# Kernel tuning notes

Hardware: AMD Instinct MI355X
Metric: run time of the kernel (lower is better)

Reference implementation:

```python
import jax, jax.numpy as jnp
import numpy as np

N_EMBD = 1024
N_HEAD = 16
HEAD_SIZE = 64


def setup_inputs() -> dict:
    key = jax.random.key(0)
    ks = jax.random.split(key, 6)
    B, T, C, H, D = 2, 2048, N_EMBD, N_HEAD, HEAD_SIZE
    s = 1.0 / np.sqrt(C)
    x = jax.random.normal(ks[0], (B, T, C), dtype=jnp.float32)
    Wq = jax.random.normal(ks[1], (H, C, D), dtype=jnp.float32) * s
    Wk = jax.random.normal(ks[2], (H, C, D), dtype=jnp.float32) * s
    Wv = jax.random.normal(ks[3], (H, C, D), dtype=jnp.float32) * s
    Wo = jax.random.normal(ks[4], (H * D, C), dtype=jnp.float32) * (1.0 / np.sqrt(H * D))
    bo = jax.random.normal(ks[5], (C,), dtype=jnp.float32) * 0.01
    return {"x": x, "Wq": Wq, "Wk": Wk, "Wv": Wv, "Wo": Wo, "bo": bo}


def reference(x, Wq, Wk, Wv, Wo, bo):
    B, T, C = x.shape
    H, _, D = Wq.shape
    # Per-head projections, batched across heads: [B,H,T,D]
    q = jnp.einsum('btc,hcd->bhtd', x, Wq)
    k = jnp.einsum('btc,hcd->bhtd', x, Wk)
    v = jnp.einsum('btc,hcd->bhtd', x, Wv)
    # NOTE: original scales by sqrt(C) = sqrt(n_embd), not sqrt(head_size)
    scale = 1.0 / jnp.sqrt(jnp.float32(C))
    att = jnp.einsum('bhtd,bhsd->bhts', q, k) * scale  # [B,H,T,T]
    causal = jnp.tril(jnp.ones((T, T), dtype=bool))
    att = jnp.where(causal, att, -jnp.inf)
    att = jax.nn.softmax(att, axis=-1)
    # dropout omitted (eval mode / deterministic reference)
    out = jnp.einsum('bhts,bhsd->bhtd', att, v)  # [B,H,T,D]
    out = out.transpose(0, 2, 1, 3).reshape(B, T, H * D)
    return out @ Wo + bo
```

## Files before the change

kernel.cpp:

```cpp
#include <hip/hip_runtime.h>
#include <hip/hip_bf16.h>


typedef __hip_bfloat16 bf16;
typedef __bf16 v8bf __attribute__((ext_vector_type(8)));
typedef float  v4f  __attribute__((ext_vector_type(4)));
typedef _Float16 v4h __attribute__((ext_vector_type(4)));
typedef unsigned long long u64;
typedef unsigned int u32;

#define MFMA16(a, b, c) __builtin_amdgcn_mfma_f32_16x16x32_bf16((a), (b), (c), 0, 0, 0)
#define MFMAH(a, b, c)  __builtin_amdgcn_mfma_f32_16x16x16f16((a), (b), (c), 0, 0, 0)

__device__ __forceinline__ bf16 f2b(float x) { return __float2bfloat16(x); }
__device__ __forceinline__ __bf16 f2braw(float x) {
  bf16 t = __float2bfloat16(x);
  return *reinterpret_cast<__bf16*>(&t);
}
__device__ __forceinline__ unsigned short f2bu(float x) {
  bf16 t = __float2bfloat16(x);
  return *reinterpret_cast<unsigned short*>(&t);
}
__device__ __forceinline__ unsigned short f2hu(float x) {
  _Float16 t = (_Float16)x;
  return *reinterpret_cast<unsigned short*>(&t);
}

__device__ __forceinline__ void load16_lds(const void* gptr, const void* lptr) {
  __builtin_amdgcn_global_load_lds(
      (const __attribute__((address_space(1))) u32*)gptr,
      (__attribute__((address_space(3))) u32*)lptr, 16, 0, 0);
}

__global__ __launch_bounds__(256) void prep_kernel(
    const float* __restrict__ x,
    const float* __restrict__ Wq, const float* __restrict__ Wk,
    const float* __restrict__ Wv, const float* __restrict__ Wo,
    bf16* __restrict__ xb, bf16* __restrict__ wt, bf16* __restrict__ wot)
{
  __shared__ float Lt[32][33];
  const int bid = blockIdx.x, tid = threadIdx.x;

  if (bid < 2048) {
    size_t i = ((size_t)bid * 256 + tid) * 8;
    float4 f0 = *(const float4*)(x + i);
    float4 f1 = *(const float4*)(x + i + 4);
    v8bf v;
    v[0] = f2braw(f0.x); v[1] = f2braw(f0.y); v[2] = f2braw(f0.z); v[3] = f2braw(f0.w);
    v[4] = f2braw(f1.x); v[5] = f2braw(f1.y); v[6] = f2braw(f1.z); v[7] = f2braw(f1.w);
    *(v8bf*)(xb + i) = v;
    return;
  }
  const int tx = tid & 31, ty = tid >> 5;
  if (bid < 5120) {
    const int idx = bid - 2048;
    const int z = idx >> 6, rem = idx & 63;
    const int p = z >> 4, h = z & 15;
    const float* ib = ((p == 0) ? Wq : (p == 1) ? Wk : Wv) + (size_t)h * 65536;
    bf16* ob = wt + (size_t)z * 65536;
    const int j0 = (rem & 1) * 32, i0 = (rem >> 1) * 32;
    #pragma unroll
    for (int r = 0; r < 4; ++r)
      Lt[ty + 8 * r][tx] = ib[(size_t)(i0 + ty + 8 * r) * 64 + j0 + tx];
    __syncthreads();
    #pragma unroll
    for (int r = 0; r < 4; ++r)
      ob[(size_t)(j0 + ty + 8 * r) * 1024 + i0 + tx] = f2b(Lt[tx][ty + 8 * r]);
  } else {
    const int idx = bid - 5120;
    const int j0 = (idx & 31) * 32, i0 = (idx >> 5) * 32;
    #pragma unroll
    for (int r = 0; r < 4; ++r)
      Lt[ty + 8 * r][tx] = Wo[(size_t)(i0 + ty + 8 * r) * 1024 + j0 + tx];
    __syncthreads();
    #pragma unroll
    for (int r = 0; r < 4; ++r)
      wot[(size_t)(j0 + ty + 8 * r) * 1024 + i0 + tx] = f2b(Lt[tx][ty + 8 * r]);
  }
}

__global__ __launch_bounds__(256) void qkv_gemm_kernel(
    const bf16* __restrict__ xb, const bf16* __restrict__ wt,
    bf16* __restrict__ qkv)
{
  __shared__ __align__(16) bf16 Ash[2][128][32];
  __shared__ __align__(16) bf16 Bsh[2][128][32];

  const int mt = blockIdx.x, nt = blockIdx.y;
  const int tid = threadIdx.x, w = tid >> 6, lane = tid & 63;
  const int ln = lane & 15, quad = lane >> 4;
  const int wm = w >> 1, wn = w & 1;
  const int m0 = mt * 128, n0 = nt * 128;

  const v4f vzero = {0.f, 0.f, 0.f, 0.f};
  v4f acc[4][4];
  #pragma unroll
  for (int mf = 0; mf < 4; ++mf)
    #pragma unroll
    for (int nf = 0; nf < 4; ++nf) acc[mf][nf] = vzero;

  const int srow = lane >> 2, sseg = (lane & 3) * 8;
  const bf16* ga = xb + (size_t)(m0 + 32 * w + srow) * 1024 + sseg;
  const bf16* gb = wt + (size_t)(n0 + 32 * w + srow) * 1024 + sseg;

  {
    load16_lds(ga,             &Ash[0][32 * w][0]);
    load16_lds(ga + 16 * 1024, &Ash[0][32 * w + 16][0]);
    load16_lds(gb,             &Bsh[0][32 * w][0]);
    load16_lds(gb + 16 * 1024, &Bsh[0][32 * w + 16][0]);
  }

  for (int kt = 0; kt < 32; ++kt) {
    const int buf = kt & 1;
    __syncthreads();

    if (kt < 31) {
      const int k0 = (kt + 1) * 32, nb = buf ^ 1;
      load16_lds(ga + k0,             &Ash[nb][32 * w][0]);
      load16_lds(ga + 16 * 1024 + k0, &Ash[nb][32 * w + 16][0]);
      load16_lds(gb + k0,             &Bsh[nb][32 * w][0]);
      load16_lds(gb + 16 * 1024 + k0, &Bsh[nb][32 * w + 16][0]);
    }

    v8bf af[4], bfv[4];
    #pragma unroll
    for (int mf = 0; mf < 4; ++mf)
      af[mf] = *(const v8bf*)&Ash[buf][wm * 64 + mf * 16 + ln][quad * 8];
    #pragma unroll
    for (int nf = 0; nf < 4; ++nf)
      bfv[nf] = *(const v8bf*)&Bsh[buf][wn * 64 + nf * 16 + ln][quad * 8];

    #pragma unroll
    for (int mf = 0; mf < 4; ++mf)
      #pragma unroll
      for (int nf = 0; nf < 4; ++nf)
        acc[mf][nf] = MFMA16(af[mf], bfv[nf], acc[mf][nf]);
  }

  const int jcol0 = n0 + wn * 64;
  const int p = jcol0 >> 10;
  const int h = (jcol0 >> 6) & 15;
  const float scale = (p == 0) ? 0.03125f : 1.0f;

  if (p < 2) {
    bf16* base = qkv + (size_t)p * 4194304 + (size_t)h * 262144;
    #pragma unroll
    for (int mf = 0; mf < 4; ++mf)
      #pragma unroll
      for (int nf = 0; nf < 4; ++nf) {
        int d = nf * 16 + ln;
        #pragma unroll
        for (int r = 0; r < 4; ++r) {
          int m = m0 + wm * 64 + mf * 16 + quad * 4 + r;
          base[(size_t)m * 64 + d] = f2b(acc[mf][nf][r] * scale);
        }
      }
  } else {
    _Float16* vb = (_Float16*)(qkv + (size_t)2 * 4194304 + (size_t)h * 262144);
    #pragma unroll
    for (int mf = 0; mf < 4; ++mf) {
      int mrow = m0 + wm * 64 + mf * 16 + quad * 4;
      int bi = mrow >> 11, t0 = mrow & 2047;
      #pragma unroll
      for (int nf = 0; nf < 4; ++nf) {
        int d = nf * 16 + ln;
        u64 pk = (u64)f2hu(acc[mf][nf][0]) |
                 ((u64)f2hu(acc[mf][nf][1]) << 16) |
                 ((u64)f2hu(acc[mf][nf][2]) << 32) |
                 ((u64)f2hu(acc[mf][nf][3]) << 48);
        *(u64*)(vb + (size_t)bi * 131072 + (size_t)d * 2048 + t0) = pk;
      }
    }
  }
}

__global__ __launch_bounds__(128) void attn_kernel(
    const bf16* __restrict__ qkv, bf16* __restrict__ att)
{
  __shared__ __align__(16) bf16     Ksh[2][2][64][32];
  __shared__ __align__(16) _Float16 Vsh[2][4][64][16];

  const int fid = blockIdx.x;
  const int mtraw = fid & 31;
  const int mt = ((fid >> 8) & 1) ? (31 - mtraw) : mtraw;
  const int grp = (fid >> 5) & 31;
  const int b = grp >> 4, h = grp & 15;
  const int row0 = mt * 64;

  const int tid = threadIdx.x, w = tid >> 6, lane = tid & 63;
  const int ln = lane & 15, quad = lane >> 4;

  const bf16* qbase = qkv + (size_t)h * 262144 + (size_t)b * 131072;
  const bf16* kbase = qbase + 4194304;
  const _Float16* vth = (const _Float16*)(qbase + 8388608);

  const int wrow = row0 + w * 32;
  v8bf aq[2][2];
  #pragma unroll
  for (int mc = 0; mc < 2; ++mc)
    #pragma unroll
    for (int ks = 0; ks < 2; ++ks)
      aq[mc][ks] = *(const v8bf*)(qbase +
          (size_t)(wrow + mc * 16 + ln) * 64 + ks * 32 + quad * 8);

  const v4f vzero = {0.f, 0.f, 0.f, 0.f};
  v4f o[2][4];
  #pragma unroll
  for (int mc = 0; mc < 2; ++mc)
    #pragma unroll
    for (int dt = 0; dt < 4; ++dt) o[mc][dt] = vzero;
  float lsum[2] = {0.f, 0.f};

  const int kb_end = mt;
  const int srow = lane >> 2, sseg = (lane & 3) * 8;

  const bf16* gk0 = kbase + (size_t)(w * 32 + srow) * 64 + sseg;
  const _Float16* gv0 = vth + (size_t)(w * 32 + (lane >> 1)) * 2048 + (lane & 1) * 8;

  #define STAGE(KB, BUF)                                                     \
    {                                                                        \
      const bf16* gk = gk0 + (size_t)(KB) * 64 * 64;                         \
      load16_lds(gk,        &Ksh[BUF][0][w * 32][0]);                        \
      load16_lds(gk + 32,   &Ksh[BUF][1][w * 32][0]);                        \
      load16_lds(gk + 1024, &Ksh[BUF][0][w * 32 + 16][0]);                   \
      load16_lds(gk + 1056, &Ksh[BUF][1][w * 32 + 16][0]);                   \
      const _Float16* gv = gv0 + (KB) * 64;                                  \
      load16_lds(gv,      &Vsh[BUF][0][w * 32][0]);                          \
      load16_lds(gv + 16, &Vsh[BUF][1][w * 32][0]);                          \
      load16_lds(gv + 32, &Vsh[BUF][2][w * 32][0]);                          \
      load16_lds(gv + 48, &Vsh[BUF][3][w * 32][0]);                          \
    }

  STAGE(0, 0)

  for (int kb = 0; kb <= kb_end; ++kb) {
    const int buf = kb & 1;
    __syncthreads();

    if (kb < kb_end) STAGE(kb + 1, buf ^ 1)

    v8bf kf[2][4];
    v4h  vf[4][4];
    #pragma unroll
    for (int tt = 0; tt < 4; ++tt) {
      kf[0][tt] = *(const v8bf*)&Ksh[buf][0][tt * 16 + ln][quad * 8];
      kf[1][tt] = *(const v8bf*)&Ksh[buf][1][tt * 16 + ln][quad * 8];
      #pragma unroll
      for (int dt = 0; dt < 4; ++dt)
        vf[tt][dt] = *(const v4h*)&Vsh[buf][tt][dt * 16 + ln][quad * 4];
    }

    const bool diag = (kb == kb_end);
    #pragma unroll
    for (int mc = 0; mc < 2; ++mc) {
      v4f st[4];
      #pragma unroll
      for (int tt = 0; tt < 4; ++tt) st[tt] = vzero;
      #pragma unroll
      for (int ks = 0; ks < 2; ++ks)
        #pragma unroll
        for (int tt = 0; tt < 4; ++tt)
          st[tt] = MFMA16(kf[ks][tt], aq[mc][ks], st[tt]);

      const int q = wrow + mc * 16 + ln;
      v4h p[4];
      #pragma unroll
      for (int tt = 0; tt < 4; ++tt) {
        #pragma unroll
        for (int r = 0; r < 4; ++r) {
          int t = kb * 64 + tt * 16 + quad * 4 + r;
          float e = (diag && t > q) ? 0.f : __expf(st[tt][r]);
          lsum[mc] += e;
          p[tt][r] = (_Float16)e;
        }
      }

      #pragma unroll
      for (int dt = 0; dt < 4; ++dt)
        #pragma unroll
        for (int tt = 0; tt < 4; ++tt)
          o[mc][dt] = MFMAH(vf[tt][dt], p[tt], o[mc][dt]);
    }
  }
  #undef STAGE

  #pragma unroll
  for (int mc = 0; mc < 2; ++mc) {
    float l = lsum[mc];
    l += __shfl_xor(l, 16);
    l += __shfl_xor(l, 32);
    float inv = 1.0f / l;
    const int m = b * 2048 + wrow + mc * 16 + ln;
    #pragma unroll
    for (int dt = 0; dt < 4; ++dt) {
      u64 pk = (u64)f2bu(o[mc][dt][0] * inv) |
               ((u64)f2bu(o[mc][dt][1] * inv) << 16) |
               ((u64)f2bu(o[mc][dt][2] * inv) << 32) |
               ((u64)f2bu(o[mc][dt][3] * inv) << 48);
      *(u64*)(att + (size_t)m * 1024 + h * 64 + dt * 16 + quad * 4) = pk;
    }
  }
}

__global__ __launch_bounds__(256) void out_gemm_kernel(
    const bf16* __restrict__ att, const bf16* __restrict__ wot,
    const float* __restrict__ bo, float* __restrict__ out)
{
  __shared__ __align__(16) bf16 Ash[2][128][32];
  __shared__ __align__(16) bf16 Bsh[2][64][32];

  const int mt = blockIdx.x, nt = blockIdx.y;
  const int tid = threadIdx.x, w = tid >> 6, lane = tid & 63;
  const int ln = lane & 15, quad = lane >> 4;
  const int wm = w >> 1, wn = w & 1;
  const int m0 = mt * 128, n0 = nt * 64;

  const v4f vzero = {0.f, 0.f, 0.f, 0.f};
  v4f acc[4][2];
  #pragma unroll
  for (int mf = 0; mf < 4; ++mf)
    #pragma unroll
    for (int nf = 0; nf < 2; ++nf) acc[mf][nf] = vzero;

  const int srow = lane >> 2, sseg = (lane & 3) * 8;
  const bf16* ga = att + (size_t)(m0 + 32 * w + srow) * 1024 + sseg;
  const bf16* gb = wot + (size_t)(n0 + 16 * w + srow) * 1024 + sseg;

  {
    load16_lds(ga,             &Ash[0][32 * w][0]);
    load16_lds(ga + 16 * 1024, &Ash[0][32 * w + 16][0]);
    load16_lds(gb,             &Bsh[0][16 * w][0]);
  }

  for (int kt = 0; kt < 32; ++kt) {
    const int buf = kt & 1;
    __syncthreads();

    if (kt < 31) {
      const int k0 = (kt + 1) * 32, nb = buf ^ 1;
      load16_lds(ga + k0,             &Ash[nb][32 * w][0]);
      load16_lds(ga + 16 * 1024 + k0, &Ash[nb][32 * w + 16][0]);
      load16_lds(gb + k0,             &Bsh[nb][16 * w][0]);
    }

    v8bf af[4], bfv[2];
    #pragma unroll
    for (int mf = 0; mf < 4; ++mf)
      af[mf] = *(const v8bf*)&Ash[buf][wm * 64 + mf * 16 + ln][quad * 8];
    #pragma unroll
    for (int nf = 0; nf < 2; ++nf)
      bfv[nf] = *(const v8bf*)&Bsh[buf][wn * 32 + nf * 16 + ln][quad * 8];

    #pragma unroll
    for (int mf = 0; mf < 4; ++mf)
      #pragma unroll
      for (int nf = 0; nf < 2; ++nf)
        acc[mf][nf] = MFMA16(af[mf], bfv[nf], acc[mf][nf]);
  }

  #pragma unroll
  for (int nf = 0; nf < 2; ++nf) {
    int j = n0 + wn * 32 + nf * 16 + ln;
    float bias = bo[j];
    #pragma unroll
    for (int mf = 0; mf < 4; ++mf)
      #pragma unroll
      for (int r = 0; r < 4; ++r) {
        int m = m0 + wm * 64 + mf * 16 + quad * 4 + r;
        out[(size_t)m * 1024 + j] = acc[mf][nf][r] + bias;
      }
  }
}

extern "C" void kernel_launch(void* const* d_in, const int* in_sizes, int n_in,
                              void* d_out, int out_size, void* d_ws, size_t ws_size,
                              hipStream_t stream) {
  const float* x  = (const float*)d_in[0];
  const float* Wq = (const float*)d_in[1];
  const float* Wk = (const float*)d_in[2];
  const float* Wv = (const float*)d_in[3];
  const float* Wo = (const float*)d_in[4];
  const float* bo = (const float*)d_in[5];
  float* out = (float*)d_out;

  bf16* xb  = (bf16*)d_ws;
  bf16* wt  = xb + 4194304;
  bf16* wot = xb + 7340032;
  bf16* qkv = xb + 8388608;
  bf16* att = xb + 20971520;

  prep_kernel<<<6144, 256, 0, stream>>>(x, Wq, Wk, Wv, Wo, xb, wt, wot);
  qkv_gemm_kernel<<<dim3(32, 24), 256, 0, stream>>>(xb, wt, qkv);
  attn_kernel<<<1024, 128, 0, stream>>>(qkv, att);
  out_gemm_kernel<<<dim3(32, 16), 256, 0, stream>>>(att, wot, bo, out);
}
```

Before: 194.6 us.

## Drop LDS staging in attention; load K/V directly to registers with 4-wave blocks

The attention kernel no longer stages K and V tiles through shared memory with barriers. Each wave now loads its K fragments straight from global memory into registers, ping-ponging two register sets to prefetch the next block, and loads V fragments directly as well. Blocks grow to 256 threads covering 128 query rows, and each wave stops at its own causal limit instead of the block's. This removes LDS traffic and __syncthreads, at the cost of redundant global/L2 reads of K/V across waves, more register pressure, and uncoalesced V loads.

New measurement: 234.6 us. 20.6% more time.

```diff
diff --git a/kernel.cpp b/kernel.cpp
--- a/kernel.cpp
+++ b/kernel.cpp
@@ -174,18 +174,14 @@
   }
 }
 
-__global__ __launch_bounds__(128) void attn_kernel(
+__global__ __launch_bounds__(256, 2) void attn_kernel(
     const bf16* __restrict__ qkv, bf16* __restrict__ att)
 {
-  __shared__ __align__(16) bf16     Ksh[2][2][64][32];
-  __shared__ __align__(16) _Float16 Vsh[2][4][64][16];
-
   const int fid = blockIdx.x;
-  const int mtraw = fid & 31;
-  const int mt = ((fid >> 8) & 1) ? (31 - mtraw) : mtraw;
-  const int grp = (fid >> 5) & 31;
-  const int b = grp >> 4, h = grp & 15;
-  const int row0 = mt * 64;
+  const int lo = fid & 255, hi = fid >> 8;
+  const int mt = hi ? (15 - (lo & 15)) : (lo & 15);
+  const int b = hi, h = (lo >> 4) & 15;
+  const int row0 = mt * 128;
 
   const int tid = threadIdx.x, w = tid >> 6, lane = tid & 63;
   const int ln = lane & 15, quad = lane >> 4;
@@ -195,6 +191,8 @@
   const _Float16* vth = (const _Float16*)(qbase + 8388608);
 
   const int wrow = row0 + w * 32;
+  const int kb_end = (wrow + 31) >> 6;
+
   v8bf aq[2][2];
   #pragma unroll
   for (int mc = 0; mc < 2; ++mc)
@@ -211,44 +209,26 @@
     for (int dt = 0; dt < 4; ++dt) o[mc][dt] = vzero;
   float lsum[2] = {0.f, 0.f};
 
-  const int kb_end = mt;
-  const int srow = lane >> 2, sseg = (lane & 3) * 8;
-
-  const bf16* gk0 = kbase + (size_t)(w * 32 + srow) * 64 + sseg;
-  const _Float16* gv0 = vth + (size_t)(w * 32 + (lane >> 1)) * 2048 + (lane & 1) * 8;
-
-  #define STAGE(KB, BUF)                                                     \
-    {                                                                        \
-      const bf16* gk = gk0 + (size_t)(KB) * 64 * 64;                         \
-      load16_lds(gk,        &Ksh[BUF][0][w * 32][0]);                        \
-      load16_lds(gk + 32,   &Ksh[BUF][1][w * 32][0]);                        \
-      load16_lds(gk + 1024, &Ksh[BUF][0][w * 32 + 16][0]);                   \
-      load16_lds(gk + 1056, &Ksh[BUF][1][w * 32 + 16][0]);                   \
-      const _Float16* gv = gv0 + (KB) * 64;                                  \
-      load16_lds(gv,      &Vsh[BUF][0][w * 32][0]);                          \
-      load16_lds(gv + 16, &Vsh[BUF][1][w * 32][0]);                          \
-      load16_lds(gv + 32, &Vsh[BUF][2][w * 32][0]);                          \
-      load16_lds(gv + 48, &Vsh[BUF][3][w * 32][0]);                          \
-    }
-
-  STAGE(0, 0)
-
-  for (int kb = 0; kb <= kb_end; ++kb) {
-    const int buf = kb & 1;
-    __syncthreads();
-
-    if (kb < kb_end) STAGE(kb + 1, buf ^ 1)
-
-    v8bf kf[2][4];
-    v4h  vf[4][4];
-    #pragma unroll
-    for (int tt = 0; tt < 4; ++tt) {
-      kf[0][tt] = *(const v8bf*)&Ksh[buf][0][tt * 16 + ln][quad * 8];
-      kf[1][tt] = *(const v8bf*)&Ksh[buf][1][tt * 16 + ln][quad * 8];
+  auto loadK = [&](v8bf (&dst)[2][4], int kb) {
+    const bf16* kp = kbase + (size_t)kb * 4096 + (size_t)ln * 64 + quad * 8;
+    #pragma unroll
+    for (int ks = 0; ks < 2; ++ks)
+      #pragma unroll
+      for (int tt = 0; tt < 4; ++tt)
+        dst[ks][tt] = *(const v8bf*)(kp + tt * 1024 + ks * 32);
+  };
+
+  auto step = [&](int kb, v8bf (&kc)[2][4], v8bf (&kn)[2][4]) {
+    v4h vf[4][4];
+    {
+      const _Float16* vp = vth + (size_t)ln * 2048 + kb * 64 + quad * 4;
       #pragma unroll
       for (int dt = 0; dt < 4; ++dt)
-        vf[tt][dt] = *(const v4h*)&Vsh[buf][tt][dt * 16 + ln][quad * 4];
-    }
+        #pragma unroll
+        for (int tt = 0; tt < 4; ++tt)
+          vf[tt][dt] = *(const v4h*)(vp + (size_t)dt * 32768 + tt * 16);
+    }
+    if (kb < kb_end) loadK(kn, kb + 1);
 
     const bool diag = (kb == kb_end);
     #pragma unroll
@@ -260,7 +240,7 @@
       for (int ks = 0; ks < 2; ++ks)
         #pragma unroll
         for (int tt = 0; tt < 4; ++tt)
-          st[tt] = MFMA16(kf[ks][tt], aq[mc][ks], st[tt]);
+          st[tt] = MFMA16(kc[ks][tt], aq[mc][ks], st[tt]);
 
       const int q = wrow + mc * 16 + ln;
       v4h p[4];
@@ -281,8 +261,14 @@
         for (int tt = 0; tt < 4; ++tt)
           o[mc][dt] = MFMAH(vf[tt][dt], p[tt], o[mc][dt]);
     }
-  }
-  #undef STAGE
+  };
+
+  v8bf kA[2][4], kB[2][4];
+  loadK(kA, 0);
+  for (int kb = 0; kb <= kb_end; kb += 2) {
+    step(kb, kA, kB);
+    if (kb + 1 <= kb_end) step(kb + 1, kB, kA);
+  }
 
   #pragma unroll
   for (int mc = 0; mc < 2; ++mc) {
@@ -391,6 +377,6 @@
 
   prep_kernel<<<6144, 256, 0, stream>>>(x, Wq, Wk, Wv, Wo, xb, wt, wot);
   qkv_gemm_kernel<<<dim3(32, 24), 256, 0, stream>>>(xb, wt, qkv);
-  attn_kernel<<<1024, 128, 0, stream>>>(qkv, att);
+  attn_kernel<<<512, 256, 0, stream>>>(qkv, att);
   out_gemm_kernel<<<dim3(32, 16), 256, 0, stream>>>(att, wot, bo, out);
 }
```
